# Performance work log

Measured on AMD Instinct MI355X. Metric: run time of the kernel, lower is better.

The kernel has to match this reference:

```python
import jax, jax.numpy as jnp
import numpy as np

D_MODEL = 1024
NUM_HEADS = 16
HEAD_DIM = D_MODEL // NUM_HEADS
HIDDEN = 4096
EPS = 1e-5


def setup_inputs() -> dict:
    key = jax.random.key(0)
    ks = jax.random.split(key, 10)
    s = 0.02
    return {
        "x": jax.random.normal(ks[0], (2, 2048, D_MODEL), dtype=jnp.float32),
        # attention projection weights stored as (in, out): y = x @ W
        "wq": jax.random.normal(ks[1], (D_MODEL, D_MODEL), dtype=jnp.float32) * s,
        "wk": jax.random.normal(ks[2], (D_MODEL, D_MODEL), dtype=jnp.float32) * s,
        "wv": jax.random.normal(ks[3], (D_MODEL, D_MODEL), dtype=jnp.float32) * s,
        "wo": jax.random.normal(ks[4], (D_MODEL, D_MODEL), dtype=jnp.float32) * s,
        # FFN
        "w1": jax.random.normal(ks[5], (D_MODEL, HIDDEN), dtype=jnp.float32) * s,
        "b1": jnp.zeros((HIDDEN,), dtype=jnp.float32),
        "w2": jax.random.normal(ks[6], (HIDDEN, D_MODEL), dtype=jnp.float32) * s,
        "b2": jnp.zeros((D_MODEL,), dtype=jnp.float32),
        # LayerNorms
        "g1": jnp.ones((D_MODEL,), dtype=jnp.float32),
        "be1": jnp.zeros((D_MODEL,), dtype=jnp.float32),
        "g2": jnp.ones((D_MODEL,), dtype=jnp.float32),
        "be2": jnp.zeros((D_MODEL,), dtype=jnp.float32),
    }


def _layernorm(x, g, b):
    mu = jnp.mean(x, axis=-1, keepdims=True)
    var = jnp.mean(jnp.square(x - mu), axis=-1, keepdims=True)
    return (x - mu) * jax.lax.rsqrt(var + EPS) * g + b


def _attention(x, wq, wk, wv, wo):
    B, S, D = x.shape
    q = (x @ wq).reshape(B, S, NUM_HEADS, HEAD_DIM)
    k = (x @ wk).reshape(B, S, NUM_HEADS, HEAD_DIM)
    v = (x @ wv).reshape(B, S, NUM_HEADS, HEAD_DIM)
    scores = jnp.einsum("bqhd,bkhd->bhqk", q, k) / jnp.sqrt(
        jnp.float32(HEAD_DIM)
    )
    causal = jnp.tril(jnp.ones((S, S), dtype=bool))
    scores = jnp.where(causal, scores, -jnp.inf)
    probs = jax.nn.softmax(scores, axis=-1)
    out = jnp.einsum("bhqk,bkhd->bqhd", probs, v).reshape(B, S, D)
    return out @ wo


def _ffn(x, w1, b1, w2, b2):
    return jax.nn.relu(x @ w1 + b1) @ w2 + b2


def reference(x, wq, wk, wv, wo, w1, b1, w2, b2, g1, be1, g2, be2):
    x = x + _attention(_layernorm(x, g1, be1), wq, wk, wv, wo)
    x = x + _ffn(_layernorm(x, g2, be2), w1, b1, w2, b2)
    return x
```

## Files before the change

kernel.cpp:

```cpp
#include <hip/hip_runtime.h>
#include <stdint.h>

typedef unsigned short bf16u;
typedef __attribute__((ext_vector_type(8))) __bf16 bf16x8;
typedef __attribute__((ext_vector_type(4))) float f32x4;
typedef __attribute__((ext_vector_type(4))) unsigned short u16x4;

typedef __attribute__((address_space(1))) void gvoid_t;
typedef __attribute__((address_space(3))) void lvoid_t;

#define SEQ 2048
#define DM 1024

__device__ __forceinline__ bf16u f2bf(float f) {
  union { float f; uint32_t u; } v; v.f = f;
  uint32_t u = v.u + 0x7fffu + ((v.u >> 16) & 1u);
  return (bf16u)(u >> 16);
}

__device__ __forceinline__ void async_copy16(const bf16u* g, const bf16u* l) {
  __builtin_amdgcn_global_load_lds((gvoid_t*)(uintptr_t)g,
                                   (lvoid_t*)(uint32_t)(uintptr_t)l,
                                   16, 0, 0);
}

#define VM_WAIT(n) asm volatile("s_waitcnt vmcnt(" #n ")" ::: "memory")
#define LGKM0()    asm volatile("s_waitcnt lgkmcnt(0)" ::: "memory")
#define BARRIER()  asm volatile("s_barrier" ::: "memory")

__global__ __launch_bounds__(256) void ln_kernel(const float* __restrict__ x,
                                                 const float* __restrict__ g,
                                                 const float* __restrict__ be,
                                                 bf16u* __restrict__ out) {
  const int row = blockIdx.x;
  const int t = threadIdx.x;
  const float4 v = ((const float4*)(x + (size_t)row * DM))[t];
  float s  = v.x + v.y + v.z + v.w;
  float ss = v.x * v.x + v.y * v.y + v.z * v.z + v.w * v.w;
#pragma unroll
  for (int m = 1; m < 64; m <<= 1) {
    s  += __shfl_xor(s, m, 64);
    ss += __shfl_xor(ss, m, 64);
  }
  __shared__ float red[2][4];
  const int wv = t >> 6, ln = t & 63;
  if (ln == 0) { red[0][wv] = s; red[1][wv] = ss; }
  __syncthreads();
  s  = red[0][0] + red[0][1] + red[0][2] + red[0][3];
  ss = red[1][0] + red[1][1] + red[1][2] + red[1][3];
  const float mu = s * (1.0f / DM);
  const float var = ss * (1.0f / DM) - mu * mu;
  const float rstd = rsqrtf(var + 1e-5f);
  const float4 gg = ((const float4*)g)[t];
  const float4 bb = ((const float4*)be)[t];
  u16x4 o;
  o[0] = f2bf((v.x - mu) * rstd * gg.x + bb.x);
  o[1] = f2bf((v.y - mu) * rstd * gg.y + bb.y);
  o[2] = f2bf((v.z - mu) * rstd * gg.z + bb.z);
  o[3] = f2bf((v.w - mu) * rstd * gg.w + bb.w);
  *(u16x4*)(out + (size_t)row * DM + t * 4) = o;
}

__global__ __launch_bounds__(256) void wtrans(const float* __restrict__ in,
                                              bf16u* __restrict__ out, int R, int C) {
  __shared__ float tile[32][33];
  const int c0 = blockIdx.x * 32, r0 = blockIdx.y * 32;
  const int tx = threadIdx.x, ty = threadIdx.y;
#pragma unroll
  for (int i = 0; i < 4; ++i)
    tile[ty + i * 8][tx] = in[(size_t)(r0 + ty + i * 8) * C + c0 + tx];
  __syncthreads();
#pragma unroll
  for (int i = 0; i < 4; ++i)
    out[(size_t)(c0 + ty + i * 8) * R + r0 + tx] = f2bf(tile[tx][ty + i * 8]);
}

__global__ __launch_bounds__(256) void wtrans4(const float* __restrict__ a,
                                               const float* __restrict__ b,
                                               const float* __restrict__ c,
                                               const float* __restrict__ d,
                                               bf16u* __restrict__ out) {
  const float* srcs[4] = {a, b, c, d};
  const float* in = srcs[blockIdx.z];
  bf16u* o = out + (size_t)blockIdx.z * 1024 * 1024;
  __shared__ float tile[32][33];
  const int c0 = blockIdx.x * 32, r0 = blockIdx.y * 32;
  const int tx = threadIdx.x, ty = threadIdx.y;
#pragma unroll
  for (int i = 0; i < 4; ++i)
    tile[ty + i * 8][tx] = in[(size_t)(r0 + ty + i * 8) * 1024 + c0 + tx];
  __syncthreads();
#pragma unroll
  for (int i = 0; i < 4; ++i)
    o[(size_t)(c0 + ty + i * 8) * 1024 + r0 + tx] = f2bf(tile[tx][ty + i * 8]);
}

__global__ __launch_bounds__(256) void vtrans(const bf16u* __restrict__ qkv,
                                              bf16u* __restrict__ vt) {
  __shared__ bf16u tile[32][33];
  const int s0 = blockIdx.x * 32;
  const int d0 = blockIdx.y * 32;
  const int bh = blockIdx.z, b = bh >> 4, h = bh & 15;
  const int tx = threadIdx.x, ty = threadIdx.y;
#pragma unroll
  for (int i = 0; i < 4; ++i)
    tile[ty + i * 8][tx] =
        qkv[(size_t)(b * SEQ + s0 + ty + i * 8) * 3072 + 2048 + h * 64 + d0 + tx];
  __syncthreads();
#pragma unroll
  for (int i = 0; i < 4; ++i)
    vt[(size_t)(bh * 64 + d0 + ty + i * 8) * SEQ + s0 + tx] = tile[tx][ty + i * 8];
}

__global__ __launch_bounds__(512, 1) void gemm256(
    const bf16u* __restrict__ A, const bf16u* __restrict__ Bt,
    int M, int N, int K,
    const float* __restrict__ bias, bf16u* __restrict__ outB, int mode) {
  __shared__ bf16u sh[2][32768];
  const int t = threadIdx.x;
  const int ln = t & 63;
  const int wv = t >> 6;
  const int col16 = ln & 15, quad = ln >> 4;
  const int wm = wv >> 2, wn = wv & 3;

  const int nbx = N >> 8;
  const int nwg = nbx * (M >> 8);
  const int cpx = nwg >> 3;
  const int bid = blockIdx.x;
  const int swz = (bid & 7) * cpx + (bid >> 3);
  const int m0 = (swz / nbx) << 8, n0 = (swz % nbx) << 8;

  const bf16u* gsrc[4][2];
  int doff[4][2];
#pragma unroll
  for (int j = 0; j < 2; ++j) {
    const int c = t + (j << 9);
    const int lr = c >> 3, slot = (c & 7) ^ (lr & 7);
    const int ra = (lr & 63) + ((lr >> 6) << 7);
    const int rb = (lr & 31) + ((lr >> 5) << 6);
    gsrc[0][j] = A  + (size_t)(m0 + ra) * K + slot * 8;
    gsrc[3][j] = A  + (size_t)(m0 + ra + 64) * K + slot * 8;
    gsrc[1][j] = Bt + (size_t)(n0 + rb) * K + slot * 8;
    gsrc[2][j] = Bt + (size_t)(n0 + rb + 32) * K + slot * 8;
    doff[0][j] = c * 8;
    doff[3][j] = 8192 + c * 8;
    doff[1][j] = 16384 + c * 8;
    doff[2][j] = 24576 + c * 8;
  }

  const int sx = col16 & 7;
  int aoffs[4][2], boffs[2][2];
#pragma unroll
  for (int i = 0; i < 4; ++i)
#pragma unroll
    for (int kc = 0; kc < 2; ++kc)
      aoffs[i][kc] = (wm * 64 + i * 16 + col16) * 64 + (((kc << 2) + quad) ^ sx) * 8;
#pragma unroll
  for (int i = 0; i < 2; ++i)
#pragma unroll
    for (int kc = 0; kc < 2; ++kc)
      boffs[i][kc] = 16384 + (wn * 32 + i * 16 + col16) * 64 + (((kc << 2) + quad) ^ sx) * 8;

  f32x4 acc[8][4] = {};
  bf16x8 Af[4][2], Bf[4][2];

  auto stage = [&](int s, int b) {
#pragma unroll
    for (int j = 0; j < 2; ++j) {
      async_copy16(gsrc[s][j], &sh[b][doff[s][j]]);
      gsrc[s][j] += 64;
    }
  };
  auto readA = [&](int b, int mh) {
#pragma unroll
    for (int i = 0; i < 4; ++i)
#pragma unroll
      for (int kc = 0; kc < 2; ++kc)
        Af[i][kc] = *(const bf16x8*)(&sh[b][mh * 8192 + aoffs[i][kc]]);
  };
  auto readB = [&](int b, int nh) {
#pragma unroll
    for (int i = 0; i < 2; ++i)
#pragma unroll
      for (int kc = 0; kc < 2; ++kc)
        Bf[nh * 2 + i][kc] = *(const bf16x8*)(&sh[b][nh * 8192 + boffs[i][kc]]);
  };
  auto mfmaQ = [&](int mh, int nh) {
#pragma unroll
    for (int kc = 0; kc < 2; ++kc)
#pragma unroll
      for (int mi = 0; mi < 4; ++mi)
#pragma unroll
        for (int nl = 0; nl < 2; ++nl)
          acc[mh * 4 + mi][nh * 2 + nl] = __builtin_amdgcn_mfma_f32_16x16x32_bf16(
              Af[mi][kc], Bf[nh * 2 + nl][kc], acc[mh * 4 + mi][nh * 2 + nl], 0, 0, 0);
  };

  const int nt = K >> 6;
  stage(0, 0); stage(1, 0); stage(2, 0); stage(3, 0);
  VM_WAIT(4);
  BARRIER();

  int bsel = 0;
  for (int kt = 0; kt < nt - 1; ++kt, bsel ^= 1) {
    const int bn = bsel ^ 1;
    readA(bsel, 0); readB(bsel, 0);
    stage(0, bn);
    BARRIER(); LGKM0();
    __builtin_amdgcn_s_setprio(1); mfmaQ(0, 0); __builtin_amdgcn_s_setprio(0);
    VM_WAIT(4); BARRIER();
    readB(bsel, 1);
    stage(1, bn);
    BARRIER(); LGKM0();
    __builtin_amdgcn_s_setprio(1); mfmaQ(0, 1); __builtin_amdgcn_s_setprio(0);
    VM_WAIT(4); BARRIER();
    readA(bsel, 1);
    stage(2, bn);
    BARRIER(); LGKM0();
    __builtin_amdgcn_s_setprio(1); mfmaQ(1, 0); __builtin_amdgcn_s_setprio(0);
    BARRIER();
    stage(3, bn);
    __builtin_amdgcn_s_setprio(1); mfmaQ(1, 1); __builtin_amdgcn_s_setprio(0);
    VM_WAIT(4); BARRIER();
  }
  readA(bsel, 0); readB(bsel, 0);
  BARRIER(); LGKM0();
  __builtin_amdgcn_s_setprio(1); mfmaQ(0, 0); __builtin_amdgcn_s_setprio(0);
  VM_WAIT(2); BARRIER();
  readB(bsel, 1);
  BARRIER(); LGKM0();
  __builtin_amdgcn_s_setprio(1); mfmaQ(0, 1); __builtin_amdgcn_s_setprio(0);
  VM_WAIT(0); BARRIER();
  readA(bsel, 1);
  LGKM0();
  __builtin_amdgcn_s_setprio(1); mfmaQ(1, 0); mfmaQ(1, 1); __builtin_amdgcn_s_setprio(0);

  float bv[4];
  if (mode == 1) {
#pragma unroll
    for (int n = 0; n < 4; ++n) bv[n] = bias[n0 + wn * 64 + n * 16 + col16];
  }
#pragma unroll
  for (int mi = 0; mi < 8; ++mi) {
#pragma unroll
    for (int n = 0; n < 4; ++n) {
      const int col = n0 + wn * 64 + n * 16 + col16;
#pragma unroll
      for (int r = 0; r < 4; ++r) {
        const int row = m0 + wm * 128 + mi * 16 + quad * 4 + r;
        float v = acc[mi][n][r];
        if (mode == 1) v = fmaxf(v + bv[n], 0.0f);
        outB[(size_t)row * N + col] = f2bf(v);
      }
    }
  }
}

__global__ __launch_bounds__(256, 3) void gemm_bt64(
    const bf16u* __restrict__ A, const bf16u* __restrict__ Bt,
    int M, int N, int K,
    const float* __restrict__ bias, const float* __restrict__ resid,
    bf16u* __restrict__ outB, float* __restrict__ outF, int mode) {
  __shared__ bf16u As0[64 * 64], As1[64 * 64];
  __shared__ bf16u Bs0[128 * 64], Bs1[128 * 64];
  const int t = threadIdx.x;
  const int ln = t & 63;
  const int wv = t >> 6;
  const int col16 = ln & 15, quad = ln >> 4;

  const int nbx = gridDim.x;
  const int nwg = nbx * gridDim.y;
  const int cpx = nwg >> 3;
  const int flat = blockIdx.y * nbx + blockIdx.x;
  const int swz = (flat & 7) * cpx + (flat >> 3);
  const int m0 = (swz / nbx) * 64, n0 = (swz % nbx) * 128;

  const bf16u* gA[2];
  const bf16u* gB[4];
#pragma unroll
  for (int j = 0; j < 2; ++j) {
    const int c = t + 256 * j, row = c >> 3, slot = (c & 7) ^ (row & 7);
    gA[j] = A + (size_t)(m0 + row) * K + slot * 8;
  }
#pragma unroll
  for (int j = 0; j < 4; ++j) {
    const int c = t + 256 * j, row = c >> 3, slot = (c & 7) ^ (row & 7);
    gB[j] = Bt + (size_t)(n0 + row) * K + slot * 8;
  }

  f32x4 acc[4][2] = {};

  auto stage = [&](bf16u* dA, bf16u* dB) {
#pragma unroll
    for (int j = 0; j < 2; ++j) {
      async_copy16(gA[j], dA + (size_t)(t + 256 * j) * 8);
      gA[j] += 64;
    }
#pragma unroll
    for (int j = 0; j < 4; ++j) {
      async_copy16(gB[j], dB + (size_t)(t + 256 * j) * 8);
      gB[j] += 64;
    }
  };
  auto compute = [&](const bf16u* sA, const bf16u* sB) {
    bf16x8 af[4][2], bfv[2][2];
#pragma unroll
    for (int mi = 0; mi < 4; ++mi) {
      const int row = mi * 16 + col16;
#pragma unroll
      for (int kc = 0; kc < 2; ++kc)
        af[mi][kc] = *(const bf16x8*)(sA + row * 64 + (((kc << 2) + quad) ^ (row & 7)) * 8);
    }
#pragma unroll
    for (int ni = 0; ni < 2; ++ni) {
      const int row = wv * 32 + ni * 16 + col16;
#pragma unroll
      for (int kc = 0; kc < 2; ++kc)
        bfv[ni][kc] = *(const bf16x8*)(sB + row * 64 + (((kc << 2) + quad) ^ (row & 7)) * 8);
    }
#pragma unroll
    for (int kc = 0; kc < 2; ++kc)
#pragma unroll
      for (int mi = 0; mi < 4; ++mi)
#pragma unroll
        for (int ni = 0; ni < 2; ++ni)
          acc[mi][ni] = __builtin_amdgcn_mfma_f32_16x16x32_bf16(af[mi][kc], bfv[ni][kc],
                                                                acc[mi][ni], 0, 0, 0);
  };

  const int niter = K >> 6;
  stage(As0, Bs0);
  for (int k = 0; k < niter; k += 2) {
    stage(As1, Bs1);
    VM_WAIT(6);
    BARRIER();
    compute(As0, Bs0);
    BARRIER();
    if (k + 2 < niter) {
      stage(As0, Bs0);
      VM_WAIT(6);
    } else {
      VM_WAIT(0);
    }
    BARRIER();
    compute(As1, Bs1);
    BARRIER();
  }

#pragma unroll
  for (int mi = 0; mi < 4; ++mi) {
#pragma unroll
    for (int ni = 0; ni < 2; ++ni) {
      const int col = n0 + wv * 32 + ni * 16 + col16;
#pragma unroll
      for (int r = 0; r < 4; ++r) {
        const int row = m0 + mi * 16 + quad * 4 + r;
        float v = acc[mi][ni][r];
        if (mode == 1 || mode == 3) v += bias[col];
        if (mode == 1) v = fmaxf(v, 0.0f);
        if (mode >= 2) {
          outF[(size_t)row * N + col] = v + resid[(size_t)row * N + col];
        } else {
          outB[(size_t)row * N + col] = f2bf(v);
        }
      }
    }
  }
}

#define PST 132
#define SCL 0.18033688f
__global__ __launch_bounds__(256, 3) void attn_kernel(const bf16u* __restrict__ qkv,
                                                      const bf16u* __restrict__ vt,
                                                      bf16u* __restrict__ out) {
  __shared__ bf16u Ks[128 * 64];
  __shared__ bf16u Vts[2 * 64 * 64];
  __shared__ bf16u pbuf[4][16 * PST];
  __shared__ float lred[4][16];
  const int t = threadIdx.x;
  const int wv = t >> 6, ln = t & 63;
  const int col = ln & 15, quad = ln >> 4;
  const int bh = blockIdx.x, b = bh >> 4, h = bh & 15;
  const int strip = 31 - blockIdx.y;
  const int q0 = strip * 64;
  const int qw = q0 + wv * 16;
  const int qmax = qw + 15;
  const int ntiles = (q0 >> 7) + 1;

  int krow[4], kslot[4], vrow[4], vsub[4], vslot[4];
  const bf16u *kl[4], *vl[4];
#pragma unroll
  for (int j = 0; j < 4; ++j) {
    const int c = t + 256 * j;
    krow[j] = c >> 3; kslot[j] = (c & 7) ^ (krow[j] & 7);
    const int rem = c & 511;
    vsub[j] = c >> 9; vrow[j] = rem >> 3; vslot[j] = (rem & 7) ^ (vrow[j] & 7);
    kl[j] = Ks + (size_t)c * 8;
    vl[j] = Vts + (size_t)c * 8;
  }

  bf16x8 qf0, qf1;
  {
    const size_t qoff = (size_t)(b * SEQ + qw + col) * 3072 + h * 64 + quad * 8;
    qf0 = *(const bf16x8*)(qkv + qoff);
    qf1 = *(const bf16x8*)(qkv + qoff + 32);
  }
  f32x4 po[4] = {};
  float ll[4] = {};

  for (int kb = 0; kb < ntiles; ++kb) {
    const int kbase = kb * 128;
#pragma unroll
    for (int j = 0; j < 4; ++j) {
      async_copy16(qkv + (size_t)(b * SEQ + kbase + krow[j]) * 3072 + 1024 + h * 64 + kslot[j] * 8, kl[j]);
      async_copy16(vt + (size_t)(bh * 64 + vrow[j]) * SEQ + kbase + vsub[j] * 64 + vslot[j] * 8, vl[j]);
    }
    asm volatile("s_waitcnt vmcnt(0)" ::: "memory");
    __syncthreads();

    if (kb < ntiles - 1) {
      f32x4 sc[8];
#pragma unroll
      for (int n = 0; n < 8; ++n) {
        const int kr = n * 16 + col;
        const bf16x8 k0 = *(const bf16x8*)(Ks + kr * 64 + (quad ^ (kr & 7)) * 8);
        const bf16x8 k1 = *(const bf16x8*)(Ks + kr * 64 + ((4 + quad) ^ (kr & 7)) * 8);
        f32x4 z = {};
        z = __builtin_amdgcn_mfma_f32_16x16x32_bf16(qf0, k0, z, 0, 0, 0);
        sc[n] = __builtin_amdgcn_mfma_f32_16x16x32_bf16(qf1, k1, z, 0, 0, 0);
      }
#pragma unroll
      for (int r = 0; r < 4; ++r) {
#pragma unroll
        for (int n = 0; n < 8; ++n) {
          const float e = exp2f(sc[n][r] * SCL);
          ll[r] += e;
          pbuf[wv][(quad * 4 + r) * PST + n * 16 + col] = f2bf(e);
        }
      }
    } else {
      f32x4 sc[8];
      bool act[8];
#pragma unroll
      for (int n = 0; n < 8; ++n) {
        act[n] = (kbase + n * 16) <= qmax;
        if (act[n]) {
          const int kr = n * 16 + col;
          const bf16x8 k0 = *(const bf16x8*)(Ks + kr * 64 + (quad ^ (kr & 7)) * 8);
          const bf16x8 k1 = *(const bf16x8*)(Ks + kr * 64 + ((4 + quad) ^ (kr & 7)) * 8);
          f32x4 z = {};
          z = __builtin_amdgcn_mfma_f32_16x16x32_bf16(qf0, k0, z, 0, 0, 0);
          sc[n] = __builtin_amdgcn_mfma_f32_16x16x32_bf16(qf1, k1, z, 0, 0, 0);
        }
      }
#pragma unroll
      for (int r = 0; r < 4; ++r) {
        const int q = qw + quad * 4 + r;
#pragma unroll
        for (int n = 0; n < 8; ++n) {
          float e = 0.0f;
          if (act[n]) {
            float v = sc[n][r] * SCL;
            v = (kbase + n * 16 + col <= q) ? v : -1e30f;
            e = exp2f(v);
          }
          ll[r] += e;
          pbuf[wv][(quad * 4 + r) * PST + n * 16 + col] = f2bf(e);
        }
      }
    }
    asm volatile("s_waitcnt lgkmcnt(0)" ::: "memory");
    bf16x8 pa[4];
#pragma unroll
    for (int kc = 0; kc < 4; ++kc)
      pa[kc] = *(const bf16x8*)(&pbuf[wv][col * PST + kc * 32 + quad * 8]);
    if (kb < ntiles - 1) {
#pragma unroll
      for (int n = 0; n < 4; ++n) {
        const int vr = n * 16 + col;
#pragma unroll
        for (int kc = 0; kc < 4; ++kc) {
          const bf16x8 vfr = *(const bf16x8*)(Vts + (kc >> 1) * 4096 + vr * 64 +
                                              (((kc & 1) * 4 + quad) ^ (vr & 7)) * 8);
          po[n] = __builtin_amdgcn_mfma_f32_16x16x32_bf16(vfr, pa[kc], po[n], 0, 0, 0);
        }
      }
    } else {
#pragma unroll
      for (int n = 0; n < 4; ++n) {
        const int vr = n * 16 + col;
#pragma unroll
        for (int kc = 0; kc < 4; ++kc)
          if (kbase + kc * 32 <= qmax) {
            const bf16x8 vfr = *(const bf16x8*)(Vts + (kc >> 1) * 4096 + vr * 64 +
                                                (((kc & 1) * 4 + quad) ^ (vr & 7)) * 8);
            po[n] = __builtin_amdgcn_mfma_f32_16x16x32_bf16(vfr, pa[kc], po[n], 0, 0, 0);
          }
      }
    }
    asm volatile("s_waitcnt lgkmcnt(0)" ::: "memory");
    __syncthreads();
  }

#pragma unroll
  for (int m = 1; m < 16; m <<= 1)
#pragma unroll
    for (int r = 0; r < 4; ++r) ll[r] += __shfl_xor(ll[r], m, 64);
  if (col == 0) {
#pragma unroll
    for (int r = 0; r < 4; ++r) lred[wv][quad * 4 + r] = ll[r];
  }
  asm volatile("s_waitcnt lgkmcnt(0)" ::: "memory");
  const float inv = 1.0f / lred[wv][col];
#pragma unroll
  for (int n = 0; n < 4; ++n) {
    u16x4 o;
#pragma unroll
    for (int r = 0; r < 4; ++r) o[r] = f2bf(po[n][r] * inv);
    *(u16x4*)(out + (size_t)(b * SEQ + qw + col) * DM + h * 64 + n * 16 + quad * 4) = o;
  }
}

extern "C" void kernel_launch(void* const* d_in, const int* in_sizes, int n_in,
                              void* d_out, int out_size, void* d_ws, size_t ws_size,
                              hipStream_t stream) {
  const float* x   = (const float*)d_in[0];
  const float* wq  = (const float*)d_in[1];
  const float* wk  = (const float*)d_in[2];
  const float* wvv = (const float*)d_in[3];
  const float* wo  = (const float*)d_in[4];
  const float* w1  = (const float*)d_in[5];
  const float* b1  = (const float*)d_in[6];
  const float* w2  = (const float*)d_in[7];
  const float* b2  = (const float*)d_in[8];
  const float* g1  = (const float*)d_in[9];
  const float* be1 = (const float*)d_in[10];
  const float* g2  = (const float*)d_in[11];
  const float* be2 = (const float*)d_in[12];
  float* out = (float*)d_out;

  char* ws = (char*)d_ws;
  bf16u* wqkv_t = (bf16u*)(ws);
  bf16u* wo_t   = (bf16u*)(ws +  6291456);
  bf16u* w1_t   = (bf16u*)(ws +  8388608);
  bf16u* w2_t   = (bf16u*)(ws + 16777216);
  bf16u* lnbuf  = (bf16u*)(ws + 25165824);
  bf16u* qkv    = (bf16u*)(ws + 33554432);
  bf16u* vtb    = (bf16u*)(ws + 58720256);
  bf16u* h1     = (bf16u*)(ws + 33554432);
  bf16u* attn   = lnbuf;

  const dim3 tb32(32, 8);
  wtrans4<<<dim3(32, 32, 4), tb32, 0, stream>>>(wq, wk, wvv, wo, wqkv_t);
  wtrans<<<dim3(128, 32), tb32, 0, stream>>>(w1, w1_t, 1024, 4096);
  wtrans<<<dim3(32, 128), tb32, 0, stream>>>(w2, w2_t, 4096, 1024);

  ln_kernel<<<4096, 256, 0, stream>>>(x, g1, be1, lnbuf);
  gemm256<<<192, 512, 0, stream>>>(lnbuf, wqkv_t, 4096, 3072, 1024,
                                   nullptr, qkv, 0);
  vtrans<<<dim3(64, 2, 32), tb32, 0, stream>>>(qkv, vtb);
  attn_kernel<<<dim3(32, 32), 256, 0, stream>>>(qkv, vtb, attn);
  gemm_bt64<<<dim3(8, 64), 256, 0, stream>>>(attn, wo_t, 4096, 1024, 1024,
                                             nullptr, x, nullptr, out, 2);
  ln_kernel<<<4096, 256, 0, stream>>>(out, g2, be2, lnbuf);
  gemm256<<<256, 512, 0, stream>>>(lnbuf, w1_t, 4096, 4096, 1024,
                                   b1, h1, 1);
  gemm_bt64<<<dim3(8, 64), 256, 0, stream>>>(h1, w2_t, 4096, 1024, 4096,
                                             b2, out, nullptr, out, 3);
}
```

Baseline: 329.2 us.

## Run FFN down-projection on the 256-tile GEMM with split-K atomic accumulation

The final FFN GEMM (4096x1024, K=4096) moves from the 64-tile kernel to the larger 256x256-tile MFMA kernel. K is split four ways so the grid reaches 256 workgroups. Each split atomically adds its partial sums into the fp32 output, which already holds the residual, and only split 0 adds the bias. The aim is higher MFMA efficiency and better CU occupancy, at the cost of atomic-add traffic and a summation order that is no longer deterministic.

```diff
diff --git a/kernel.cpp b/kernel.cpp
--- a/kernel.cpp
+++ b/kernel.cpp
@@ -115,7 +115,8 @@
 __global__ __launch_bounds__(512, 1) void gemm256(
     const bf16u* __restrict__ A, const bf16u* __restrict__ Bt,
     int M, int N, int K,
-    const float* __restrict__ bias, bf16u* __restrict__ outB, int mode) {
+    const float* __restrict__ bias, bf16u* __restrict__ outB,
+    float* __restrict__ outF, int mode, int lgS) {
   __shared__ bf16u sh[2][32768];
   const int t = threadIdx.x;
   const int ln = t & 63;
@@ -124,11 +125,15 @@
   const int wm = wv >> 2, wn = wv & 3;
 
   const int nbx = N >> 8;
-  const int nwg = nbx * (M >> 8);
+  const int nwg = (nbx * (M >> 8)) << lgS;
   const int cpx = nwg >> 3;
   const int bid = blockIdx.x;
   const int swz = (bid & 7) * cpx + (bid >> 3);
-  const int m0 = (swz / nbx) << 8, n0 = (swz % nbx) << 8;
+  const int split = swz & ((1 << lgS) - 1);
+  const int tile = swz >> lgS;
+  const int m0 = (tile / nbx) << 8, n0 = (tile % nbx) << 8;
+  const int Ks = K >> lgS;
+  const size_t koff = (size_t)split * Ks;
 
   const bf16u* gsrc[4][2];
   int doff[4][2];
@@ -138,10 +143,10 @@
     const int lr = c >> 3, slot = (c & 7) ^ (lr & 7);
     const int ra = (lr & 63) + ((lr >> 6) << 7);
     const int rb = (lr & 31) + ((lr >> 5) << 6);
-    gsrc[0][j] = A  + (size_t)(m0 + ra) * K + slot * 8;
-    gsrc[3][j] = A  + (size_t)(m0 + ra + 64) * K + slot * 8;
-    gsrc[1][j] = Bt + (size_t)(n0 + rb) * K + slot * 8;
-    gsrc[2][j] = Bt + (size_t)(n0 + rb + 32) * K + slot * 8;
+    gsrc[0][j] = A  + (size_t)(m0 + ra) * K + koff + slot * 8;
+    gsrc[3][j] = A  + (size_t)(m0 + ra + 64) * K + koff + slot * 8;
+    gsrc[1][j] = Bt + (size_t)(n0 + rb) * K + koff + slot * 8;
+    gsrc[2][j] = Bt + (size_t)(n0 + rb + 32) * K + koff + slot * 8;
     doff[0][j] = c * 8;
     doff[3][j] = 8192 + c * 8;
     doff[1][j] = 16384 + c * 8;
@@ -196,7 +201,7 @@
               Af[mi][kc], Bf[nh * 2 + nl][kc], acc[mh * 4 + mi][nh * 2 + nl], 0, 0, 0);
   };
 
-  const int nt = K >> 6;
+  const int nt = Ks >> 6;
   stage(0, 0); stage(1, 0); stage(2, 0); stage(3, 0);
   VM_WAIT(4);
   BARRIER();
@@ -235,6 +240,26 @@
   LGKM0();
   __builtin_amdgcn_s_setprio(1); mfmaQ(1, 0); mfmaQ(1, 1); __builtin_amdgcn_s_setprio(0);
 
+  if (mode == 4) {
+    float bv[4] = {0.f, 0.f, 0.f, 0.f};
+    if (split == 0 && bias) {
+#pragma unroll
+      for (int n = 0; n < 4; ++n) bv[n] = bias[n0 + wn * 64 + n * 16 + col16];
+    }
+#pragma unroll
+    for (int mi = 0; mi < 8; ++mi) {
+#pragma unroll
+      for (int n = 0; n < 4; ++n) {
+        const int col = n0 + wn * 64 + n * 16 + col16;
+#pragma unroll
+        for (int r = 0; r < 4; ++r) {
+          const int row = m0 + wm * 128 + mi * 16 + quad * 4 + r;
+          unsafeAtomicAdd(&outF[(size_t)row * N + col], acc[mi][n][r] + bv[n]);
+        }
+      }
+    }
+    return;
+  }
   float bv[4];
   if (mode == 1) {
 #pragma unroll
@@ -557,14 +582,14 @@
 
   ln_kernel<<<4096, 256, 0, stream>>>(x, g1, be1, lnbuf);
   gemm256<<<192, 512, 0, stream>>>(lnbuf, wqkv_t, 4096, 3072, 1024,
-                                   nullptr, qkv, 0);
+                                   nullptr, qkv, nullptr, 0, 0);
   vtrans<<<dim3(64, 2, 32), tb32, 0, stream>>>(qkv, vtb);
   attn_kernel<<<dim3(32, 32), 256, 0, stream>>>(qkv, vtb, attn);
   gemm_bt64<<<dim3(8, 64), 256, 0, stream>>>(attn, wo_t, 4096, 1024, 1024,
                                              nullptr, x, nullptr, out, 2);
   ln_kernel<<<4096, 256, 0, stream>>>(out, g2, be2, lnbuf);
   gemm256<<<256, 512, 0, stream>>>(lnbuf, w1_t, 4096, 4096, 1024,
-                                   b1, h1, 1);
-  gemm_bt64<<<dim3(8, 64), 256, 0, stream>>>(h1, w2_t, 4096, 1024, 4096,
-                                             b2, out, nullptr, out, 3);
-}
+                                   b1, h1, nullptr, 1, 0);
+  gemm256<<<256, 512, 0, stream>>>(h1, w2_t, 4096, 1024, 4096,
+                                   b2, nullptr, out, 4, 2);
+}
```

After: 353.8 us. +7.5%, slower.

## Fuse V transpose into QKV GEMM epilogue and triple-buffer the narrow GEMM

Applied to the files above, without the earlier changes.

The QKV GEMM now writes the V columns directly in transposed per-head layout (mode 5), which removes the separate vtrans kernel and its extra read and write of V. Separately, gemm_bt64 moves from double to triple buffering with a two-stage-ahead prefetch and a per-iteration loop. The extra LDS this needs lowers the occupancy hint from 3 to 2 blocks per CU. The transposed store writes 4 contiguous elements per lane, so it is less coalesced than the old tiled transpose, and the added buffering trades occupancy for deeper prefetch.

```diff
diff --git a/kernel.cpp b/kernel.cpp
--- a/kernel.cpp
+++ b/kernel.cpp
@@ -95,27 +95,11 @@
     o[(size_t)(c0 + ty + i * 8) * 1024 + r0 + tx] = f2bf(tile[tx][ty + i * 8]);
 }
 
-__global__ __launch_bounds__(256) void vtrans(const bf16u* __restrict__ qkv,
-                                              bf16u* __restrict__ vt) {
-  __shared__ bf16u tile[32][33];
-  const int s0 = blockIdx.x * 32;
-  const int d0 = blockIdx.y * 32;
-  const int bh = blockIdx.z, b = bh >> 4, h = bh & 15;
-  const int tx = threadIdx.x, ty = threadIdx.y;
-#pragma unroll
-  for (int i = 0; i < 4; ++i)
-    tile[ty + i * 8][tx] =
-        qkv[(size_t)(b * SEQ + s0 + ty + i * 8) * 3072 + 2048 + h * 64 + d0 + tx];
-  __syncthreads();
-#pragma unroll
-  for (int i = 0; i < 4; ++i)
-    vt[(size_t)(bh * 64 + d0 + ty + i * 8) * SEQ + s0 + tx] = tile[tx][ty + i * 8];
-}
-
 __global__ __launch_bounds__(512, 1) void gemm256(
     const bf16u* __restrict__ A, const bf16u* __restrict__ Bt,
     int M, int N, int K,
-    const float* __restrict__ bias, bf16u* __restrict__ outB, int mode) {
+    const float* __restrict__ bias, bf16u* __restrict__ outB,
+    bf16u* __restrict__ vt, int mode) {
   __shared__ bf16u sh[2][32768];
   const int t = threadIdx.x;
   const int ln = t & 63;
@@ -235,6 +219,23 @@
   LGKM0();
   __builtin_amdgcn_s_setprio(1); mfmaQ(1, 0); mfmaQ(1, 1); __builtin_amdgcn_s_setprio(0);
 
+  if (mode == 5 && n0 >= 2048) {
+#pragma unroll
+    for (int mi = 0; mi < 8; ++mi) {
+#pragma unroll
+      for (int n = 0; n < 4; ++n) {
+        const int col = n0 + wn * 64 + n * 16 + col16;
+        const int hh = (col - 2048) >> 6, d = (col - 2048) & 63;
+        const int row_base = m0 + wm * 128 + mi * 16 + quad * 4;
+        const int bb = row_base >> 11, s = row_base & 2047;
+        u16x4 o;
+#pragma unroll
+        for (int r = 0; r < 4; ++r) o[r] = f2bf(acc[mi][n][r]);
+        *(u16x4*)(vt + (size_t)((bb * 16 + hh) * 64 + d) * SEQ + s) = o;
+      }
+    }
+    return;
+  }
   float bv[4];
   if (mode == 1) {
 #pragma unroll
@@ -256,13 +257,13 @@
   }
 }
 
-__global__ __launch_bounds__(256, 3) void gemm_bt64(
+__global__ __launch_bounds__(256, 2) void gemm_bt64(
     const bf16u* __restrict__ A, const bf16u* __restrict__ Bt,
     int M, int N, int K,
     const float* __restrict__ bias, const float* __restrict__ resid,
     bf16u* __restrict__ outB, float* __restrict__ outF, int mode) {
-  __shared__ bf16u As0[64 * 64], As1[64 * 64];
-  __shared__ bf16u Bs0[128 * 64], Bs1[128 * 64];
+  __shared__ bf16u As0[64 * 64], As1[64 * 64], As2[64 * 64];
+  __shared__ bf16u Bs0[128 * 64], Bs1[128 * 64], Bs2[128 * 64];
   const int t = threadIdx.x;
   const int ln = t & 63;
   const int wv = t >> 6;
@@ -329,22 +330,24 @@
   };
 
   const int niter = K >> 6;
-  stage(As0, Bs0);
-  for (int k = 0; k < niter; k += 2) {
-    stage(As1, Bs1);
-    VM_WAIT(6);
-    BARRIER();
-    compute(As0, Bs0);
-    BARRIER();
+  bf16u *a0 = As0, *a1 = As1, *a2 = As2;
+  bf16u *b0 = Bs0, *b1 = Bs1, *b2 = Bs2;
+  stage(a0, b0);
+  stage(a1, b1);
+  for (int k = 0; k < niter; ++k) {
     if (k + 2 < niter) {
-      stage(As0, Bs0);
+      stage(a2, b2);
+      VM_WAIT(12);
+    } else if (k + 1 < niter) {
       VM_WAIT(6);
     } else {
       VM_WAIT(0);
     }
     BARRIER();
-    compute(As1, Bs1);
+    compute(a0, b0);
     BARRIER();
+    bf16u* ta = a0; a0 = a1; a1 = a2; a2 = ta;
+    bf16u* tb = b0; b0 = b1; b1 = b2; b2 = tb;
   }
 
 #pragma unroll
@@ -557,14 +560,13 @@
 
   ln_kernel<<<4096, 256, 0, stream>>>(x, g1, be1, lnbuf);
   gemm256<<<192, 512, 0, stream>>>(lnbuf, wqkv_t, 4096, 3072, 1024,
-                                   nullptr, qkv, 0);
-  vtrans<<<dim3(64, 2, 32), tb32, 0, stream>>>(qkv, vtb);
+                                   nullptr, qkv, vtb, 5);
   attn_kernel<<<dim3(32, 32), 256, 0, stream>>>(qkv, vtb, attn);
   gemm_bt64<<<dim3(8, 64), 256, 0, stream>>>(attn, wo_t, 4096, 1024, 1024,
                                              nullptr, x, nullptr, out, 2);
   ln_kernel<<<4096, 256, 0, stream>>>(out, g2, be2, lnbuf);
   gemm256<<<256, 512, 0, stream>>>(lnbuf, w1_t, 4096, 4096, 1024,
-                                   b1, h1, 1);
+                                   b1, h1, nullptr, 1);
   gemm_bt64<<<dim3(8, 64), 256, 0, stream>>>(h1, w2_t, 4096, 1024, 4096,
                                              b2, out, nullptr, out, 3);
 }
```

Result: no change. 326.8 us (-0.7%).
